# Performance work log

Measured on AMD Instinct MI355X. Metric: run time of the kernel, lower is better.

## Reference

```python
import jax, jax.numpy as jnp
import numpy as np

NEG_SLOPE = 0.02

def _leaky(x):
    return jnp.where(x >= 0, x, NEG_SLOPE * x)

def _conv1d(x, w, b):
    # x: (B, Cin, T), w: (Cout, Cin, 3) torch layout; SAME padding, stride 1
    y = jax.lax.conv_general_dilated(x, w, window_strides=(1,), padding=[(1, 1)],
                                     dimension_numbers=('NCH', 'OIH', 'NCH'))
    return y + b[None, :, None]

def setup_inputs() -> dict:
    key = jax.random.key(0)
    ks = iter(jax.random.split(key, 40))
    B, T, NA, S, NE, NID = 32768, 9, 64, 32, 53, 5000
    def rn(shape, scale=0.1):
        return (jax.random.normal(next(ks), shape, dtype=jnp.float32) * scale)
    inp = {
        'x': jax.random.normal(next(ks), (B, T, NA), dtype=jnp.float32),
        'identity_id': jax.random.randint(next(ks), (B,), 0, NID, dtype=jnp.int32),
        'cw1': rn((32, 64, 3)), 'cb1': rn((32,)),
        'cw2': rn((64, 32, 3)), 'cb2': rn((64,)),
        'cw3': rn((128, 64, 3)), 'cb3': rn((128,)),
        'cw4': rn((64, 128, 3)), 'cb4': rn((64,)),
        'fw1': rn((128, 64)), 'fb1': rn((128,)),
        'fw2': rn((64, 128)), 'fb2': rn((64,)),
        'fw3': rn((32, 64)), 'fb3': rn((32,)),
        'aw1': rn((16, 32, 3)), 'ab1': rn((16,)),
        'aw2': rn((8, 16, 3)), 'ab2': rn((8,)),
        'aw3': rn((4, 8, 3)), 'ab3': rn((4,)),
        'aw4': rn((2, 4, 3)), 'ab4': rn((2,)),
        'aw5': rn((1, 2, 3)), 'ab5': rn((1,)),
        'lw': rn((9, 9)), 'lb': rn((9,)),
        'mapping': jax.random.normal(next(ks), (1, NID, NE, S), dtype=jnp.float32),
    }
    return inp

def reference(x, identity_id, cw1, cb1, cw2, cb2, cw3, cb3, cw4, cb4,
              fw1, fb1, fw2, fb2, fw3, fb3,
              aw1, ab1, aw2, ab2, aw3, ab3, aw4, ab4, aw5, ab5,
              lw, lb, mapping):
    B, T, _ = x.shape          # (B, 9, 64)
    S = fw3.shape[0]           # subspace_dim = 32
    h = jnp.transpose(x, (0, 2, 1))  # (B, 64, 9)
    h = _leaky(_conv1d(h, cw1, cb1))
    h = _leaky(_conv1d(h, cw2, cb2))
    h = _leaky(_conv1d(h, cw3, cb3))
    h = _leaky(_conv1d(h, cw4, cb4))  # (B, 64, 9)
    # faithful to torch: reshape (B,64,9) -> (B*9, 1, 64) row-major (mixes C and T)
    h = h.reshape(B * T, 64)
    h = _leaky(h @ fw1.T + fb1)
    h = _leaky(h @ fw2.T + fb2)
    h = jnp.tanh(h @ fw3.T + fb3)        # (B*T, S)
    rs_T = h.reshape(B, T, S).transpose(0, 2, 1)  # (B, S, T)
    a = _leaky(_conv1d(rs_T, aw1, ab1))
    a = _leaky(_conv1d(a, aw2, ab2))
    a = _leaky(_conv1d(a, aw3, ab3))
    a = _leaky(_conv1d(a, aw4, ab4))
    a = _leaky(_conv1d(a, aw5, ab5))     # (B, 1, T)
    logits = a.reshape(B, T) @ lw.T + lb
    att = jax.nn.softmax(logits, axis=1)            # (B, T)
    sub = jnp.einsum('bst,bt->bs', rs_T, att)       # (B, S)
    m = mapping[0][identity_id]                     # (B, n_expression, S)
    return 10.0 * jnp.einsum('bes,bs->be', m, sub)  # (B, n_expression)
```

## Files before the change

### kernel.cpp

```cpp
#include <hip/hip_runtime.h>
#include <hip/hip_bf16.h>
#include <math.h>

#define THREADS 256
#define WAVES 4
#define NB 8
#define MROWS (NB*9)
#define MT 5

#define P1SZ 20736
#define P2SZ 10496
#define POOLSZ (P1SZ + P2SZ)

typedef __attribute__((ext_vector_type(8))) short bf16x8;
typedef __attribute__((ext_vector_type(4))) float f32x4;

__device__ __forceinline__ float leaky(float x){ return fmaxf(x, 0.02f*x); }
__device__ __forceinline__ float fast_tanh(float x){
  float e = __expf(2.f*x);
  return 1.f - 2.f/(e + 1.f);
}

__device__ __forceinline__ unsigned short f2bf(float f){
  union { float f; unsigned u; } v; v.f = f;
  unsigned r = (v.u + 0x7FFFu + ((v.u >> 16) & 1u)) >> 16;
  return (unsigned short)r;
}
__device__ __forceinline__ float bf2f(unsigned short h){
  union { unsigned u; float f; } v; v.u = ((unsigned)h) << 16;
  return v.f;
}
__device__ __forceinline__ unsigned pack2bf(float a, float b){
  float2 t; t.x = a; t.y = b;
  __hip_bfloat162 h = __float22bfloat162_rn(t);
  union { __hip_bfloat162 h; unsigned u; } c; c.h = h;
  return c.u;
}

template<int L2R>
__device__ __forceinline__ unsigned swz(unsigned b){
  if constexpr (L2R < 0) return b;
  else return b ^ (((b >> L2R) & 7u) << 4);
}

__device__ __forceinline__ f32x4 mfma16(bf16x8 a, bf16x8 b, f32x4 c){
  return __builtin_amdgcn_mfma_f32_16x16x32_bf16(a, b, c, 0, 0, 0);
}

#define WB_C1 0
#define WB_C2 6144
#define WB_C3 12288
#define WB_C4 36864
#define WB_F1 61440
#define WB_F2 69632
#define WB_F3 77824
#define WB_A1 79872
#define WB_A2 81408
#define WB_A3 82432
#define WB_A4 82944
#define WB_A5 83456
#define WP_TOTAL 83968

__global__ void pack_weights(
    const float* __restrict__ cw1, const float* __restrict__ cw2,
    const float* __restrict__ cw3, const float* __restrict__ cw4,
    const float* __restrict__ fw1, const float* __restrict__ fw2,
    const float* __restrict__ fw3, const float* __restrict__ aw1,
    const float* __restrict__ aw2, const float* __restrict__ aw3,
    const float* __restrict__ aw4, const float* __restrict__ aw5,
    short* __restrict__ wp)
{
  int g = blockIdx.x*256 + threadIdx.x;
  if (g >= WP_TOTAL) return;
  const float* w; int base, l2cp, cinw, cout, KS; bool conv;
  if      (g < WB_C2){ w=cw1; base=WB_C1; l2cp=6; cinw=64;  cout=32;  KS=6;  conv=true; }
  else if (g < WB_C3){ w=cw2; base=WB_C2; l2cp=5; cinw=32;  cout=64;  KS=3;  conv=true; }
  else if (g < WB_C4){ w=cw3; base=WB_C3; l2cp=6; cinw=64;  cout=128; KS=6;  conv=true; }
  else if (g < WB_F1){ w=cw4; base=WB_C4; l2cp=7; cinw=128; cout=64;  KS=12; conv=true; }
  else if (g < WB_F2){ w=fw1; base=WB_F1; l2cp=6; cinw=64;  cout=128; KS=2;  conv=false; }
  else if (g < WB_F3){ w=fw2; base=WB_F2; l2cp=7; cinw=128; cout=64;  KS=4;  conv=false; }
  else if (g < WB_A1){ w=fw3; base=WB_F3; l2cp=6; cinw=64;  cout=32;  KS=2;  conv=false; }
  else if (g < WB_A2){ w=aw1; base=WB_A1; l2cp=5; cinw=32;  cout=16;  KS=3;  conv=true; }
  else if (g < WB_A3){ w=aw2; base=WB_A2; l2cp=4; cinw=16;  cout=8;   KS=2;  conv=true; }
  else if (g < WB_A4){ w=aw3; base=WB_A3; l2cp=3; cinw=8;   cout=4;   KS=1;  conv=true; }
  else if (g < WB_A5){ w=aw4; base=WB_A4; l2cp=3; cinw=4;   cout=2;   KS=1;  conv=true; }
  else               { w=aw5; base=WB_A5; l2cp=3; cinw=2;   cout=1;   KS=1;  conv=true; }
  int local = g - base;
  int frag = local >> 9;
  int lane = (local >> 3) & 63;
  int j    = local & 7;
  int nt = frag / KS, ks = frag - nt*KS;
  int hi = lane >> 4, lo = lane & 15;
  int k = ks*32 + hi*8 + j;
  int n = nt*16 + lo;
  float v = 0.f;
  if (n < cout){
    if (conv){
      int dt = k >> l2cp, ci = k & ((1<<l2cp)-1);
      if (dt < 3 && ci < cinw) v = w[((size_t)n*cinw + ci)*3 + dt];
    } else {
      v = w[(size_t)n*cinw + k];
    }
  }
  wp[g] = (short)f2bf(v);
}

template<int CINP, int CINW, int COUT, int STORE_CH, int KS, int MYNT,
         int L2RI, int L2RO, bool IN_CONV, int OUT_MODE, int ACT,
         int LBASE, int GOFF, bool PACKED>
__device__ __forceinline__ void mfma_layer(
    const short* __restrict__ wp, const float* __restrict__ w,
    const float* __restrict__ bias, const char* __restrict__ inb,
    char* __restrict__ outb, int tid)
{
  constexpr int NT = (COUT + 15)/16;
  constexpr int NTG = (NT + MYNT - 1)/MYNT;
  constexpr int L2CINP = (CINP==8?3:CINP==16?4:CINP==32?5:CINP==64?6:7);
  constexpr bool HOIST = (MYNT <= 2);
  const int wave = tid >> 6, lane = tid & 63;
  const int hi = lane >> 4, lo = lane & 15;

  int nt0, mlo, mhi;
  if constexpr (NTG >= WAVES){
    nt0 = (wave % NTG)*MYNT; mlo = 0; mhi = MT;
  } else {
    constexpr int WPN = WAVES/NTG;
    int seg = wave / NTG; int g = wave - seg*NTG;
    nt0 = g*MYNT; mlo = (MT*seg)/WPN; mhi = (MT*(seg+1))/WPN;
  }

  const int k0h = hi*8;

  bf16x8 Bf[MYNT][KS];
  #pragma unroll
  for (int nt = 0; nt < MYNT; ++nt){
    #pragma unroll
    for (int ks = 0; ks < KS; ++ks){
      if constexpr (PACKED){
        Bf[nt][ks] = *(const bf16x8*)(wp + LBASE + (((nt0+nt)*KS + ks) << 9) + lane*8);
      } else {
        bf16x8 r;
        int n = (nt0+nt)*16 + lo;
        #pragma unroll
        for (int j = 0; j < 8; ++j){
          int k = ks*32 + k0h + j;
          float v = 0.f;
          if (n < COUT){
            if constexpr (IN_CONV){
              int dt = k >> L2CINP, ci = k & (CINP-1);
              if (dt < 3 && ci < CINW) v = w[((size_t)n*CINW + ci)*3 + dt];
            } else {
              v = w[(size_t)n*CINP + k];
            }
          }
          r[j] = (short)f2bf(v);
        }
        Bf[nt][ks] = r;
      }
    }
  }

  float bvh[MYNT][4];
  if constexpr (HOIST){
    #pragma unroll
    for (int nt = 0; nt < MYNT; ++nt){
      int n0 = (nt0+nt)*16 + hi*4;
      if constexpr (COUT >= 4){
        if (n0 < COUT){
          const float4 b4 = *(const float4*)(bias + n0);
          bvh[nt][0]=b4.x; bvh[nt][1]=b4.y; bvh[nt][2]=b4.z; bvh[nt][3]=b4.w;
        } else { bvh[nt][0]=bvh[nt][1]=bvh[nt][2]=bvh[nt][3]=0.f; }
      } else {
        #pragma unroll
        for (int r = 0; r < 4; ++r) bvh[nt][r] = (n0 + r < COUT) ? bias[n0+r] : 0.f;
      }
    }
  }

  auto store_out = [&](int nt, const f32x4& a, int R, int bl2, int t2){
    const int n0 = (nt0+nt)*16 + hi*4;
    float bv[4];
    if constexpr (HOIST){
      bv[0]=bvh[nt][0]; bv[1]=bvh[nt][1]; bv[2]=bvh[nt][2]; bv[3]=bvh[nt][3];
    } else {
      if constexpr (COUT >= 4){
        if (n0 < COUT){
          const float4 b4 = *(const float4*)(bias + n0);
          bv[0]=b4.x; bv[1]=b4.y; bv[2]=b4.z; bv[3]=b4.w;
        } else { bv[0]=bv[1]=bv[2]=bv[3]=0.f; }
      } else {
        #pragma unroll
        for (int r = 0; r < 4; ++r) bv[r] = (n0 + r < COUT) ? bias[n0+r] : 0.f;
      }
    }
    if constexpr (OUT_MODE == 2){
      if (R < MROWS){
        #pragma unroll
        for (int r = 0; r < 4; ++r){
          float vr = leaky(a[r] + bv[r]);
          unsigned byte = (unsigned)((bl2*576 + (n0+r)*9 + t2)*2);
          *(short*)(outb + swz<L2RO>(byte)) = (short)f2bf(vr);
        }
      }
    } else if constexpr (OUT_MODE == 3){
      if (hi == 0){
        float vr0 = a[0] + bv[0];
        float vr = (ACT==0) ? leaky(vr0) : fast_tanh(vr0);
        *(short*)(outb + (unsigned)(R*2)) = (short)f2bf(vr);
      }
    } else {
      if (n0 < STORE_CH){
        float v[4];
        #pragma unroll
        for (int r = 0; r < 4; ++r){
          float vr0 = a[r] + bv[r];
          float vr = (ACT==0) ? leaky(vr0) : fast_tanh(vr0);
          if constexpr (STORE_CH > COUT){ if (n0 + r >= COUT) vr = 0.f; }
          v[r] = vr;
        }
        unsigned byte = (unsigned)R*(unsigned)(STORE_CH*2) + (unsigned)(n0*2);
        uint2 pk; pk.x = pack2bf(v[0], v[1]); pk.y = pack2bf(v[2], v[3]);
        *(uint2*)(outb + swz<L2RO>(byte)) = pk;
      }
    }
  };

  for (int m = mlo; m < mhi; ++m){
    int R = m*16 + lo;
    int bl2 = (int)((unsigned)R/9u);
    int tl = R - bl2*9;

    f32x4 acc[MYNT];
    #pragma unroll
    for (int nt = 0; nt < MYNT; ++nt)
      acc[nt] = (f32x4){0.f, 0.f, 0.f, 0.f};

    #pragma unroll
    for (int ks = 0; ks < KS; ++ks){
      bf16x8 Af;
      if constexpr (IN_CONV){
        int k0 = ks*32 + k0h;
        int dtv = k0 >> L2CINP;
        unsigned ra = swz<L2RI>((unsigned)(((R-1)*CINP + k0) << 1));
        bool ok = ((unsigned)(tl + dtv - 1) < 9u) && (dtv < 3);
        unsigned addr = ok ? ra : (unsigned)GOFF;
        Af = *(const bf16x8*)(inb + addr);
      } else {
        unsigned byte0 = (unsigned)((R*CINP + ks*32 + k0h) << 1);
        Af = *(const bf16x8*)(inb + swz<L2RI>(byte0));
      }
      #pragma unroll
      for (int nt = 0; nt < MYNT; ++nt)
        acc[nt] = mfma16(Bf[nt][ks], Af, acc[nt]);
    }
    #pragma unroll
    for (int nt = 0; nt < MYNT; ++nt) store_out(nt, acc[nt], R, bl2, tl);
  }
}

template<bool PACKED>
__global__ __launch_bounds__(THREADS, 5)
void fused_expr_kernel(
    const float* __restrict__ x, const int* __restrict__ ident,
    const float* __restrict__ cw1, const float* __restrict__ cb1,
    const float* __restrict__ cw2, const float* __restrict__ cb2,
    const float* __restrict__ cw3, const float* __restrict__ cb3,
    const float* __restrict__ cw4, const float* __restrict__ cb4,
    const float* __restrict__ fw1, const float* __restrict__ fb1,
    const float* __restrict__ fw2, const float* __restrict__ fb2,
    const float* __restrict__ fw3, const float* __restrict__ fb3,
    const float* __restrict__ aw1, const float* __restrict__ ab1,
    const float* __restrict__ aw2, const float* __restrict__ ab2,
    const float* __restrict__ aw3, const float* __restrict__ ab3,
    const float* __restrict__ aw4, const float* __restrict__ ab4,
    const float* __restrict__ aw5, const float* __restrict__ ab5,
    const float* __restrict__ lw,  const float* __restrict__ lb,
    const float* __restrict__ mapping, const short* __restrict__ wp,
    float* __restrict__ out)
{
  __shared__ __align__(16) char pool[POOLSZ];

  char* P1 = pool;
  char* P2 = pool + P1SZ;

  float* logits_s = (float*)(P2 + 7168);
  float* att_s    = (float*)(P2 + 7456);
  float* sub_s    = (float*)(P2 + 7744);

  const int tid = threadIdx.x;
  const int b0 = blockIdx.x * NB;
  const int p  = tid >> 3;
  const int bl = tid & 7;

  const uint2 z2 = {0u, 0u};

  {
    const float4* xb4 = (const float4*)(x + (size_t)b0 * 576);
    for (int i = tid; i < NB*144; i += THREADS){
      int b = i / 144; int rem = i - b*144;
      int t = rem >> 4; int c4 = rem & 15;
      float4 v = xb4[i];
      uint2 pk;
      pk.x = pack2bf(v.x, v.y);
      pk.y = pack2bf(v.z, v.w);
      unsigned byte = (unsigned)(((b*9 + t)*64 + c4*4)*2);
      *(uint2*)(P2 + swz<7>(byte)) = pk;
    }
    for (int i = tid; i < 128; i += THREADS){
      int rr = 72 + (i >> 4); int c4 = i & 15;
      unsigned byte = (unsigned)((rr*64 + c4*4)*2);
      *(uint2*)(P2 + swz<7>(byte)) = z2;
    }
    if (tid < 12){
      int g = tid >> 2, o = (tid & 3)*8;
      char* dst = (g==0) ? (P2 + 10240 + o) : (g==1) ? (P1 + 5120 + o) : (P1 + 20480 + o);
      *(uint2*)dst = z2;
    }
  }
  __syncthreads();

  mfma_layer<64, 64, 32, 32, 6, 1, 7, 6, true, 0, 0, WB_C1, 10240, PACKED>(wp, cw1, cb1, P2, P1, tid); __syncthreads();
  mfma_layer<32, 32, 64, 64, 3, 2, 6, 7, true, 0, 0, WB_C2, 5120,  PACKED>(wp, cw2, cb2, P1, P2, tid); __syncthreads();
  mfma_layer<64, 64,128,128, 6, 2, 7, 8, true, 0, 0, WB_C3, 10240, PACKED>(wp, cw3, cb3, P2, P1, tid); __syncthreads();
  mfma_layer<128,128,64, 64,12, 1, 8, 7, true, 2, 0, WB_C4, 20480, PACKED>(wp, cw4, cb4, P1, P2, tid); __syncthreads();
  mfma_layer<64, 64,128,128, 2, 4, 7, 8, false,0, 0, WB_F1, 0,     PACKED>(wp, fw1, fb1, P2, P1, tid); __syncthreads();
  mfma_layer<128,128,64, 64, 4, 2, 8, 7, false,0, 0, WB_F2, 0,     PACKED>(wp, fw2, fb2, P1, P2, tid); __syncthreads();
  mfma_layer<64, 64, 32, 32, 2, 2, 7, 6, false,0, 1, WB_F3, 0,     PACKED>(wp, fw3, fb3, P2, P1, tid);
  if (tid < 4) *(uint2*)(P1 + 5120 + tid*8) = z2;
  __syncthreads();

  char* rs = P1;
  char* a1 = P2;
  char* a2 = P1 + 8192;
  char* a3 = P2 + 4096;
  char* a4 = P1 + 12288;
  char* a5 = P2 + 6144;

  mfma_layer<32, 32, 16, 16, 3, 1, 6, 5, true, 0, 0, WB_A1, 5120, PACKED>(wp, aw1, ab1, rs, a1, tid);
  if (tid < 4) *(uint2*)(a1 + 2560 + tid*8) = z2;
  __syncthreads();
  mfma_layer<16, 16,  8,  8, 2, 1, 5,-1, true, 0, 0, WB_A2, 2560, PACKED>(wp, aw2, ab2, a1, a2, tid);
  if (tid < 4) *(uint2*)(a2 + 1280 + tid*8) = z2;
  __syncthreads();
  mfma_layer< 8,  8,  4,  8, 1, 1,-1,-1, true, 0, 0, WB_A3, 1280, PACKED>(wp, aw3, ab3, a2, a3, tid);
  if (tid < 4) *(uint2*)(a3 + 1280 + tid*8) = z2;
  __syncthreads();
  mfma_layer< 8,  4,  2,  8, 1, 1,-1,-1, true, 0, 0, WB_A4, 1280, PACKED>(wp, aw4, ab4, a3, a4, tid);
  if (tid < 4) *(uint2*)(a4 + 1280 + tid*8) = z2;
  __syncthreads();
  mfma_layer< 8,  2,  1,  1, 1, 1,-1,-1, true, 3, 0, WB_A5, 1280, PACKED>(wp, aw5, ab5, a4, a5, tid);
  __syncthreads();

  if (p < 9){
    float acc = lb[p];
    #pragma unroll
    for (int t = 0; t < 9; ++t)
      acc = fmaf(lw[p*9 + t], bf2f(*(const unsigned short*)(a5 + (bl*9 + t)*2)), acc);
    logits_s[bl*9 + p] = acc;
  }
  __syncthreads();

  if (p == 0){
    float m = -1e30f;
    #pragma unroll
    for (int t = 0; t < 9; ++t) m = fmaxf(m, logits_s[bl*9 + t]);
    float s = 0.f, ex[9];
    #pragma unroll
    for (int t = 0; t < 9; ++t){ ex[t] = __expf(logits_s[bl*9 + t] - m); s += ex[t]; }
    float inv = 1.f / s;
    #pragma unroll
    for (int t = 0; t < 9; ++t) att_s[bl*9 + t] = ex[t]*inv;
  }
  __syncthreads();

  {
    int s = p;
    float acc = 0.f;
    #pragma unroll
    for (int t = 0; t < 9; ++t){
      unsigned byte = (unsigned)(((bl*9 + t)*32 + s)*2);
      acc = fmaf(bf2f(*(const unsigned short*)(rs + swz<6>(byte))), att_s[bl*9 + t], acc);
    }
    sub_s[bl*32 + s] = acc;
  }
  __syncthreads();

  {
    const int b = b0 + bl;
    const size_t id = (size_t)ident[b];
    const float* mb = mapping + id*53*32;
    const float* subp = &sub_s[bl*32];
    for (int e = p; e < 53; e += 32){
      const float4* mrow4 = (const float4*)(mb + e*32);
      float acc = 0.f;
      #pragma unroll
      for (int s4 = 0; s4 < 8; ++s4){
        float4 mv = mrow4[s4];
        acc = fmaf(mv.x, subp[s4*4+0], acc);
        acc = fmaf(mv.y, subp[s4*4+1], acc);
        acc = fmaf(mv.z, subp[s4*4+2], acc);
        acc = fmaf(mv.w, subp[s4*4+3], acc);
      }
      out[(size_t)b*53 + e] = 10.f*acc;
    }
  }
}

extern "C" void kernel_launch(void* const* d_in, const int* in_sizes, int n_in,
                              void* d_out, int out_size, void* d_ws, size_t ws_size,
                              hipStream_t stream) {
  const float* x    = (const float*)d_in[0];
  const int*   ident= (const int*)  d_in[1];
  const float* cw1  = (const float*)d_in[2];  const float* cb1 = (const float*)d_in[3];
  const float* cw2  = (const float*)d_in[4];  const float* cb2 = (const float*)d_in[5];
  const float* cw3  = (const float*)d_in[6];  const float* cb3 = (const float*)d_in[7];
  const float* cw4  = (const float*)d_in[8];  const float* cb4 = (const float*)d_in[9];
  const float* fw1  = (const float*)d_in[10]; const float* fb1 = (const float*)d_in[11];
  const float* fw2  = (const float*)d_in[12]; const float* fb2 = (const float*)d_in[13];
  const float* fw3  = (const float*)d_in[14]; const float* fb3 = (const float*)d_in[15];
  const float* aw1  = (const float*)d_in[16]; const float* ab1 = (const float*)d_in[17];
  const float* aw2  = (const float*)d_in[18]; const float* ab2 = (const float*)d_in[19];
  const float* aw3  = (const float*)d_in[20]; const float* ab3 = (const float*)d_in[21];
  const float* aw4  = (const float*)d_in[22]; const float* ab4 = (const float*)d_in[23];
  const float* aw5  = (const float*)d_in[24]; const float* ab5 = (const float*)d_in[25];
  const float* lw   = (const float*)d_in[26]; const float* lb  = (const float*)d_in[27];
  const float* mapping = (const float*)d_in[28];

  const int B = 32768;
  dim3 grid(B / NB), block(THREADS);

  const bool packed = ws_size >= (size_t)(WP_TOTAL * 2);
  short* wpk = (short*)d_ws;

  if (packed){
    pack_weights<<<dim3(WP_TOTAL/256), dim3(256), 0, stream>>>(
        cw1, cw2, cw3, cw4, fw1, fw2, fw3, aw1, aw2, aw3, aw4, aw5, wpk);
    fused_expr_kernel<true><<<grid, block, 0, stream>>>(
        x, ident, cw1, cb1, cw2, cb2, cw3, cb3, cw4, cb4,
        fw1, fb1, fw2, fb2, fw3, fb3,
        aw1, ab1, aw2, ab2, aw3, ab3, aw4, ab4, aw5, ab5,
        lw, lb, mapping, wpk, (float*)d_out);
  } else {
    fused_expr_kernel<false><<<grid, block, 0, stream>>>(
        x, ident, cw1, cb1, cw2, cb2, cw3, cb3, cw4, cb4,
        fw1, fb1, fw2, fb2, fw3, fb3,
        aw1, ab1, aw2, ab2, aw3, ab3, aw4, ab4, aw5, ab5,
        lw, lb, mapping, wpk, (float*)d_out);
  }
}
```

Before: 131.2 us.

## Run attention tail per-wave with scalar convs and wave-local sync

Replaces the tiny attention conv layers a2–a5 (previously padded MFMA layers separated by block-wide barriers) with scalar FMA convolutions. Each wave now handles two batch rows in its own LDS scratch region. Block-level __syncthreads between the tail stages become wave-local lgkmcnt waits, so waves no longer stall on each other. The softmax, attention pooling and mapping projection are also reorganised per wave. In exchange, less parallelism is used per stage, and the code relies on wave-synchronous LDS visibility.

```diff
diff --git a/kernel.cpp b/kernel.cpp
--- a/kernel.cpp
+++ b/kernel.cpp
@@ -11,6 +11,10 @@
 #define P1SZ 20736
 #define P2SZ 10496
 #define POOLSZ (P1SZ + P2SZ)
+#define WS_STRIDE 1280
+
+#define WSYNC() do { __asm__ volatile("s_waitcnt lgkmcnt(0)" ::: "memory"); \
+                     __builtin_amdgcn_sched_barrier(0); } while(0)
 
 typedef __attribute__((ext_vector_type(8))) short bf16x8;
 typedef __attribute__((ext_vector_type(4))) float f32x4;
@@ -202,12 +206,6 @@
           *(short*)(outb + swz<L2RO>(byte)) = (short)f2bf(vr);
         }
       }
-    } else if constexpr (OUT_MODE == 3){
-      if (hi == 0){
-        float vr0 = a[0] + bv[0];
-        float vr = (ACT==0) ? leaky(vr0) : fast_tanh(vr0);
-        *(short*)(outb + (unsigned)(R*2)) = (short)f2bf(vr);
-      }
     } else {
       if (n0 < STORE_CH){
         float v[4];
@@ -255,6 +253,44 @@
     }
     #pragma unroll
     for (int nt = 0; nt < MYNT; ++nt) store_out(nt, acc[nt], R, bl2, tl);
+  }
+}
+
+template<int CIN, int COUT>
+__device__ __forceinline__ void tail_conv(const float* __restrict__ w,
+    const float* __restrict__ bias, const char* inp, char* outp, int lane)
+{
+  const int b = lane >> 5, l5 = lane & 31;
+  const int co = l5 >> 2, tg = l5 & 3;
+  if (l5 < COUT*4){
+    int tstart = (tg==0) ? 0 : (2*tg+1);
+    int tcnt   = (tg==0) ? 3 : 2;
+    float bv = bias[co];
+    float acc[3]; acc[0]=bv; acc[1]=bv; acc[2]=bv;
+    for (int ci = 0; ci < CIN; ++ci){
+      float tap[5];
+      #pragma unroll
+      for (int k = 0; k < 5; ++k){
+        float v = 0.f;
+        if (k < tcnt + 2){
+          int idx = tstart + k;
+          v = bf2f(*(const unsigned short*)(inp + (b*11*CIN + idx*CIN + ci)*2));
+        }
+        tap[k] = v;
+      }
+      const float* wq = w + (co*CIN + ci)*3;
+      float w0 = wq[0], w1 = wq[1], w2 = wq[2];
+      #pragma unroll
+      for (int j = 0; j < 3; ++j)
+        acc[j] = fmaf(w0, tap[j], fmaf(w1, tap[j+1], fmaf(w2, tap[j+2], acc[j])));
+    }
+    #pragma unroll
+    for (int j = 0; j < 3; ++j){
+      if (j < tcnt){
+        int t = tstart + j;
+        *(short*)(outp + (b*11*COUT + (t+1)*COUT + co)*2) = (short)f2bf(leaky(acc[j]));
+      }
+    }
   }
 }
 
@@ -283,14 +319,8 @@
   char* P1 = pool;
   char* P2 = pool + P1SZ;
 
-  float* logits_s = (float*)(P2 + 7168);
-  float* att_s    = (float*)(P2 + 7456);
-  float* sub_s    = (float*)(P2 + 7744);
-
   const int tid = threadIdx.x;
   const int b0 = blockIdx.x * NB;
-  const int p  = tid >> 3;
-  const int bl = tid & 7;
 
   const uint2 z2 = {0u, 0u};
 
@@ -331,77 +361,133 @@
 
   char* rs = P1;
   char* a1 = P2;
-  char* a2 = P1 + 8192;
-  char* a3 = P2 + 4096;
-  char* a4 = P1 + 12288;
-  char* a5 = P2 + 6144;
 
   mfma_layer<32, 32, 16, 16, 3, 1, 6, 5, true, 0, 0, WB_A1, 5120, PACKED>(wp, aw1, ab1, rs, a1, tid);
-  if (tid < 4) *(uint2*)(a1 + 2560 + tid*8) = z2;
   __syncthreads();
-  mfma_layer<16, 16,  8,  8, 2, 1, 5,-1, true, 0, 0, WB_A2, 2560, PACKED>(wp, aw2, ab2, a1, a2, tid);
-  if (tid < 4) *(uint2*)(a2 + 1280 + tid*8) = z2;
-  __syncthreads();
-  mfma_layer< 8,  8,  4,  8, 1, 1,-1,-1, true, 0, 0, WB_A3, 1280, PACKED>(wp, aw3, ab3, a2, a3, tid);
-  if (tid < 4) *(uint2*)(a3 + 1280 + tid*8) = z2;
-  __syncthreads();
-  mfma_layer< 8,  4,  2,  8, 1, 1,-1,-1, true, 0, 0, WB_A4, 1280, PACKED>(wp, aw4, ab4, a3, a4, tid);
-  if (tid < 4) *(uint2*)(a4 + 1280 + tid*8) = z2;
-  __syncthreads();
-  mfma_layer< 8,  2,  1,  1, 1, 1,-1,-1, true, 3, 0, WB_A5, 1280, PACKED>(wp, aw5, ab5, a4, a5, tid);
-  __syncthreads();
-
-  if (p < 9){
-    float acc = lb[p];
-    #pragma unroll
-    for (int t = 0; t < 9; ++t)
-      acc = fmaf(lw[p*9 + t], bf2f(*(const unsigned short*)(a5 + (bl*9 + t)*2)), acc);
-    logits_s[bl*9 + p] = acc;
-  }
-  __syncthreads();
-
-  if (p == 0){
-    float m = -1e30f;
-    #pragma unroll
-    for (int t = 0; t < 9; ++t) m = fmaxf(m, logits_s[bl*9 + t]);
-    float s = 0.f, ex[9];
-    #pragma unroll
-    for (int t = 0; t < 9; ++t){ ex[t] = __expf(logits_s[bl*9 + t] - m); s += ex[t]; }
-    float inv = 1.f / s;
-    #pragma unroll
-    for (int t = 0; t < 9; ++t) att_s[bl*9 + t] = ex[t]*inv;
-  }
-  __syncthreads();
 
   {
-    int s = p;
-    float acc = 0.f;
-    #pragma unroll
-    for (int t = 0; t < 9; ++t){
-      unsigned byte = (unsigned)(((bl*9 + t)*32 + s)*2);
-      acc = fmaf(bf2f(*(const unsigned short*)(rs + swz<6>(byte))), att_s[bl*9 + t], acc);
-    }
-    sub_s[bl*32 + s] = acc;
-  }
-  __syncthreads();
-
-  {
-    const int b = b0 + bl;
-    const size_t id = (size_t)ident[b];
-    const float* mb = mapping + id*53*32;
-    const float* subp = &sub_s[bl*32];
-    for (int e = p; e < 53; e += 32){
-      const float4* mrow4 = (const float4*)(mb + e*32);
+    const int lane = tid & 63;
+    const int wave = tid >> 6;
+    const int b_loc = lane >> 5;
+    const int l5 = lane & 31;
+    const int bg = wave*2 + b_loc;
+    const int rowb = bg*9;
+
+    char* ws = P1 + 8192 + wave*WS_STRIDE;
+    char* a2s = ws;
+    char* a3s = ws + 384;
+    char* a4s = ws + 576;
+    char* a5s = ws + 672;
+    float* lg  = (float*)(ws + 720);
+    float* att = (float*)(ws + 800);
+    float* subs= (float*)(ws + 896);
+
+    for (int i = lane; i < WS_STRIDE/4; i += 64) ((unsigned*)ws)[i] = 0u;
+    WSYNC();
+
+    {
+      const int co = l5 >> 2, tg = l5 & 3;
+      int tstart = (tg==0) ? 0 : (2*tg+1);
+      int tcnt   = (tg==0) ? 3 : 2;
+      float bv = ab2[co];
+      float acc[3]; acc[0]=bv; acc[1]=bv; acc[2]=bv;
+      for (int ci = 0; ci < 16; ++ci){
+        float tap[5];
+        #pragma unroll
+        for (int k = 0; k < 5; ++k){
+          int tt = tstart - 1 + k;
+          float v = 0.f;
+          if (k < tcnt + 2 && (unsigned)tt < 9u){
+            unsigned byte = (unsigned)(((rowb + tt)*16 + ci)*2);
+            v = bf2f(*(const unsigned short*)(a1 + swz<5>(byte)));
+          }
+          tap[k] = v;
+        }
+        const float* wq = aw2 + (co*16 + ci)*3;
+        float w0 = wq[0], w1 = wq[1], w2 = wq[2];
+        #pragma unroll
+        for (int j = 0; j < 3; ++j)
+          acc[j] = fmaf(w0, tap[j], fmaf(w1, tap[j+1], fmaf(w2, tap[j+2], acc[j])));
+      }
+      #pragma unroll
+      for (int j = 0; j < 3; ++j){
+        if (j < tcnt){
+          int t = tstart + j;
+          *(short*)(a2s + (b_loc*88 + (t+1)*8 + co)*2) = (short)f2bf(leaky(acc[j]));
+        }
+      }
+    }
+    WSYNC();
+
+    tail_conv<8, 4>(aw3, ab3, a2s, a3s, lane);
+    WSYNC();
+    tail_conv<4, 2>(aw4, ab4, a3s, a4s, lane);
+    WSYNC();
+    tail_conv<2, 1>(aw5, ab5, a4s, a5s, lane);
+    WSYNC();
+
+    if (l5 < 9){
+      int o = l5;
+      float acc = lb[o];
+      #pragma unroll
+      for (int t = 0; t < 9; ++t)
+        acc = fmaf(lw[o*9 + t], bf2f(*(const unsigned short*)(a5s + (b_loc*11 + t+1)*2)), acc);
+      lg[b_loc*9 + o] = acc;
+    }
+    WSYNC();
+
+    if (l5 == 0){
+      float m = -1e30f;
+      #pragma unroll
+      for (int t = 0; t < 9; ++t) m = fmaxf(m, lg[b_loc*9 + t]);
+      float s = 0.f, ex[9];
+      #pragma unroll
+      for (int t = 0; t < 9; ++t){ ex[t] = __expf(lg[b_loc*9 + t] - m); s += ex[t]; }
+      float inv = 1.f / s;
+      #pragma unroll
+      for (int t = 0; t < 9; ++t) att[b_loc*9 + t] = ex[t]*inv;
+    }
+    WSYNC();
+
+    {
       float acc = 0.f;
       #pragma unroll
-      for (int s4 = 0; s4 < 8; ++s4){
-        float4 mv = mrow4[s4];
-        acc = fmaf(mv.x, subp[s4*4+0], acc);
-        acc = fmaf(mv.y, subp[s4*4+1], acc);
-        acc = fmaf(mv.z, subp[s4*4+2], acc);
-        acc = fmaf(mv.w, subp[s4*4+3], acc);
-      }
-      out[(size_t)b*53 + e] = 10.f*acc;
+      for (int t = 0; t < 9; ++t){
+        unsigned byte = (unsigned)(((rowb + t)*32 + l5)*2);
+        acc = fmaf(bf2f(*(const unsigned short*)(rs + swz<6>(byte))), att[b_loc*9 + t], acc);
+      }
+      subs[b_loc*32 + l5] = acc;
+    }
+    WSYNC();
+
+    {
+      float sv[32];
+      const float4* sp4 = (const float4*)(subs + b_loc*32);
+      #pragma unroll
+      for (int q = 0; q < 8; ++q){
+        float4 v = sp4[q];
+        sv[q*4+0]=v.x; sv[q*4+1]=v.y; sv[q*4+2]=v.z; sv[q*4+3]=v.w;
+      }
+      const int b = b0 + bg;
+      const size_t id = (size_t)ident[b];
+      const float* mb = mapping + id*53*32;
+      #pragma unroll
+      for (int h = 0; h < 2; ++h){
+        int e = h*32 + l5;
+        if (e < 53){
+          const float4* mrow4 = (const float4*)(mb + e*32);
+          float acc = 0.f;
+          #pragma unroll
+          for (int s4 = 0; s4 < 8; ++s4){
+            float4 mv = mrow4[s4];
+            acc = fmaf(mv.x, sv[s4*4+0], acc);
+            acc = fmaf(mv.y, sv[s4*4+1], acc);
+            acc = fmaf(mv.z, sv[s4*4+2], acc);
+            acc = fmaf(mv.w, sv[s4*4+3], acc);
+          }
+          out[(size_t)b*53 + e] = 10.f*acc;
+        }
+      }
     }
   }
 }
```

New measurement: 199.5 us. 1.52x slower.
